# Performance work log

Measured on AMD Instinct MI355X. Metric: run time of the kernel, lower is better.

The kernel has to match this reference:

```python
import jax, jax.numpy as jnp
import numpy as np

B, S, D, H, G = 4, 2048, 1024, 16, 32
HD = D // H
LN_EPS = 1e-5


def _lin_init(key, fan_in, fan_out):
    kw, kb = jax.random.split(key)
    bound = 1.0 / np.sqrt(fan_in)
    W = jax.random.uniform(kw, (fan_in, fan_out), jnp.float32, -bound, bound)
    b = jax.random.uniform(kb, (fan_out,), jnp.float32, -bound, bound)
    return W, b


def setup_inputs() -> dict:
    key = jax.random.key(0)
    ks = jax.random.split(key, 9)
    x = jax.random.normal(ks[0], (B, S, D), jnp.float32)
    geo_features = jax.random.normal(ks[1], (B, G), jnp.float32)
    Wq, bq = _lin_init(ks[2], D, D)
    Wk, bk = _lin_init(ks[3], D, D)
    Wv, bv = _lin_init(ks[4], D, D)
    Wo, bo = _lin_init(ks[5], D, D)
    ge_W1, ge_b1 = _lin_init(ks[6], G, D)
    ln_g = jnp.ones((D,), jnp.float32)
    ln_b = jnp.zeros((D,), jnp.float32)
    ge_W2, ge_b2 = _lin_init(ks[7], D, D)
    gm_W, gm_b = _lin_init(ks[8], D, H)
    return dict(x=x, geo_features=geo_features, Wq=Wq, bq=bq, Wk=Wk, bk=bk,
                Wv=Wv, bv=bv, Wo=Wo, bo=bo, ge_W1=ge_W1, ge_b1=ge_b1,
                ln_g=ln_g, ln_b=ln_b, ge_W2=ge_W2, ge_b2=ge_b2,
                gm_W=gm_W, gm_b=gm_b)


def reference(x, geo_features, Wq, bq, Wk, bk, Wv, bv, Wo, bo,
              ge_W1, ge_b1, ln_g, ln_b, ge_W2, ge_b2, gm_W, gm_b):
    # QKV projections -> (B, H, S, HD)
    def split_heads(t):
        return t.reshape(B, S, H, HD).transpose(0, 2, 1, 3)
    Q = split_heads(x @ Wq + bq)
    K = split_heads(x @ Wk + bk)
    V = split_heads(x @ Wv + bv)

    # geo encoder: Linear -> LayerNorm -> ReLU -> Linear
    h = geo_features @ ge_W1 + ge_b1                      # (B, D)
    mu = jnp.mean(h, axis=-1, keepdims=True)
    var = jnp.mean(jnp.square(h - mu), axis=-1, keepdims=True)
    h = (h - mu) / jnp.sqrt(var + LN_EPS) * ln_g + ln_b
    h = jax.nn.relu(h)
    geo_encoded = h @ ge_W2 + ge_b2                       # (B, D)
    geo_mod = jax.nn.sigmoid(geo_encoded @ gm_W + gm_b)   # (B, H)

    scale = 1.0 / np.sqrt(HD)
    scores = jnp.einsum('bhqd,bhkd->bhqk', Q, K) * scale  # (B, H, S, S)
    scores = scores * (1.0 + geo_mod[:, :, None, None])
    attn = jax.nn.softmax(scores, axis=-1)                # dropout in eval mode: identity
    ctx = jnp.einsum('bhqk,bhkd->bhqd', attn, V)          # (B, H, S, HD)
    ctx = ctx.transpose(0, 2, 1, 3).reshape(B, S, D)
    out = ctx @ Wo + bo
    return out, attn
```

## Files before the change

kernel.cpp:

```cpp
#include <hip/hip_runtime.h>

typedef __attribute__((ext_vector_type(8))) short bf16x8;
typedef __attribute__((ext_vector_type(4))) float f32x4;
typedef __attribute__((ext_vector_type(4))) unsigned short us4;
typedef unsigned short u16;

#define MB (1024*1024)

#define WAITV(N) asm volatile("s_waitcnt vmcnt(" #N ")" ::: "memory")
#define WAITL0() asm volatile("s_waitcnt lgkmcnt(0)" ::: "memory")
#define BAR()    __builtin_amdgcn_s_barrier()
#define SCHEDB() __builtin_amdgcn_sched_barrier(0)

__device__ __forceinline__ u16 f2bf(float f) {
    unsigned u = __float_as_uint(f);
    unsigned r = (u + 0x7fffu + ((u >> 16) & 1u)) >> 16;
    return (u16)r;
}

__device__ __forceinline__ unsigned cvtpk(float a, float b) {
    unsigned r;
    asm("v_cvt_pk_bf16_f32 %0, %1, %2" : "=v"(r) : "v"(a), "v"(b));
    return r;
}

__device__ __forceinline__ f32x4 mfma16(bf16x8 a, bf16x8 b, f32x4 c) {
    return __builtin_amdgcn_mfma_f32_16x16x32_bf16(a, b, c, 0, 0, 0);
}

__device__ __forceinline__ void gload16(const void* g, void* l) {
    __builtin_amdgcn_global_load_lds(
        (__attribute__((address_space(1))) void*)(unsigned long long)g,
        (__attribute__((address_space(3))) void*)l, 16, 0, 0);
}

__global__ __launch_bounds__(256) void k_cvtx(const float* __restrict__ x, u16* __restrict__ xb) {
    const long long i = (long long)blockIdx.x * 256 + threadIdx.x;
    const float4* xp = (const float4*)x;
    float4 a = xp[i*2], b = xp[i*2+1];
    bf16x8 o;
    o[0]=(short)f2bf(a.x); o[1]=(short)f2bf(a.y); o[2]=(short)f2bf(a.z); o[3]=(short)f2bf(a.w);
    o[4]=(short)f2bf(b.x); o[5]=(short)f2bf(b.y); o[6]=(short)f2bf(b.z); o[7]=(short)f2bf(b.w);
    *(bf16x8*)&xb[i*8] = o;
}

__global__ __launch_bounds__(256) void k_wtcvt(const float* __restrict__ W0, const float* __restrict__ W1,
                                               const float* __restrict__ W2, const float* __restrict__ W3,
                                               u16* __restrict__ wt) {
    __shared__ float tl[32][33];
    const int t = threadIdx.x, z = blockIdx.z;
    const float* W = (z==0)?W0:(z==1)?W1:(z==2)?W2:W3;
    const int k0 = blockIdx.x*32, n0 = blockIdx.y*32;
    const int r = t >> 3, c4 = (t & 7) * 4;
    float4 v = *(const float4*)&W[(long long)(k0+r)*1024 + n0 + c4];
    tl[r][c4] = v.x; tl[r][c4+1] = v.y; tl[r][c4+2] = v.z; tl[r][c4+3] = v.w;
    __syncthreads();
    us4 ov;
    ov[0] = f2bf(tl[c4+0][r]); ov[1] = f2bf(tl[c4+1][r]);
    ov[2] = f2bf(tl[c4+2][r]); ov[3] = f2bf(tl[c4+3][r]);
    *(us4*)&wt[((long long)z << 20) + (long long)(n0+r)*1024 + k0 + c4] = ov;
}

__global__ __launch_bounds__(1024) void k_geo1(const float* __restrict__ geo, const float* __restrict__ W1,
                                               const float* __restrict__ b1, const float* __restrict__ lng,
                                               const float* __restrict__ lnb, float* __restrict__ hr) {
    const int b = blockIdx.x, j = threadIdx.x;
    float acc = b1[j];
    #pragma unroll 8
    for (int g = 0; g < 32; ++g) acc += geo[b*32+g] * W1[(long long)g*1024 + j];
    float s1 = acc, s2 = acc*acc;
    #pragma unroll
    for (int m = 1; m < 64; m <<= 1) { s1 += __shfl_xor(s1, m); s2 += __shfl_xor(s2, m); }
    __shared__ float r1[16], r2[16];
    __shared__ float mu_s, rv_s;
    const int wid = threadIdx.x >> 6, lid = threadIdx.x & 63;
    if (lid == 0) { r1[wid] = s1; r2[wid] = s2; }
    __syncthreads();
    if (threadIdx.x == 0) {
        float S1 = 0.f, S2 = 0.f;
        for (int i = 0; i < 16; ++i) { S1 += r1[i]; S2 += r2[i]; }
        float mu = S1 / 1024.f;
        float var = S2 / 1024.f - mu*mu;
        mu_s = mu; rv_s = rsqrtf(var + 1e-5f);
    }
    __syncthreads();
    float hv = (acc - mu_s) * rv_s * lng[j] + lnb[j];
    hr[b*1024 + j] = fmaxf(hv, 0.f);
}

__global__ __launch_bounds__(256) void k_geo2(const float* __restrict__ hr, const float* __restrict__ W2,
                                              const float* __restrict__ b2, float* __restrict__ ge) {
    const int b = blockIdx.x >> 2;
    const int j = (blockIdx.x & 3)*256 + threadIdx.x;
    __shared__ float hs[1024];
    #pragma unroll
    for (int i = 0; i < 4; ++i) hs[threadIdx.x*4 + i] = hr[b*1024 + threadIdx.x*4 + i];
    __syncthreads();
    float acc = b2[j];
    #pragma unroll 8
    for (int d = 0; d < 1024; ++d) acc += hs[d] * W2[(long long)d*1024 + j];
    ge[b*1024 + j] = acc;
}

__global__ __launch_bounds__(64) void k_geo3(const float* __restrict__ ge, const float* __restrict__ gmW,
                                             const float* __restrict__ gmb, float* __restrict__ qs) {
    const int t = threadIdx.x;
    const int b = t >> 4, hh = t & 15;
    float acc = gmb[hh];
    #pragma unroll 8
    for (int d = 0; d < 1024; ++d) acc += ge[b*1024 + d] * gmW[d*16 + hh];
    qs[t] = 0.125f * (1.f + 1.f/(1.f + __expf(-acc)));
}

__global__ __launch_bounds__(256) void k_qkv_gemm(const u16* __restrict__ xb, const u16* __restrict__ wtq,
                                                  const float* __restrict__ bq, const float* __restrict__ bk,
                                                  const float* __restrict__ bv, u16* __restrict__ outq) {
    __shared__ u16 lA[128*64];
    __shared__ u16 lB[128*64];
    const int t = threadIdx.x, z = blockIdx.z;
    const int m0 = blockIdx.y * 128, n0 = blockIdx.x * 128;
    const u16* wt = wtq + (long long)z * (1024*1024);
    const float* bias = (z==0) ? bq : (z==1) ? bk : bv;
    u16* out = outq + (long long)z * 8388608;
    const int w = t >> 6, l = t & 63, lm = l & 15, lg = l >> 4;
    const int wr = (w >> 1) * 64, wc = (w & 1) * 64;
    f32x4 acc[4][4] = {};
    const char* gA = (const char*)xb + (long long)(m0 + (t>>3))*2048 + (t&7)*16;
    const char* gB = (const char*)wt + (long long)(n0 + (t>>3))*2048 + (t&7)*16;
    char* lAp = (char*)lA + t*16;
    char* lBp = (char*)lB + t*16;
    for (int k0 = 0; k0 < 1024; k0 += 64) {
        #pragma unroll
        for (int i = 0; i < 4; ++i) {
            gload16(gA + (long long)i*32*2048, lAp + i*4096);
            gload16(gB + (long long)i*32*2048, lBp + i*4096);
        }
        gA += 128; gB += 128;
        __syncthreads();
        #pragma unroll
        for (int kk = 0; kk < 2; ++kk) {
            bf16x8 af[4], bfr[4];
            #pragma unroll
            for (int mi = 0; mi < 4; ++mi)
                af[mi] = *(const bf16x8*)((const char*)lA + (wr + mi*16 + lm)*128 + kk*64 + lg*16);
            #pragma unroll
            for (int ni = 0; ni < 4; ++ni)
                bfr[ni] = *(const bf16x8*)((const char*)lB + (wc + ni*16 + lm)*128 + kk*64 + lg*16);
            #pragma unroll
            for (int mi = 0; mi < 4; ++mi)
                #pragma unroll
                for (int ni = 0; ni < 4; ++ni)
                    acc[mi][ni] = mfma16(af[mi], bfr[ni], acc[mi][ni]);
        }
        __syncthreads();
    }
    #pragma unroll
    for (int ni = 0; ni < 4; ++ni) {
        const int n = n0 + wc + ni*16 + lm;
        const float bn = bias[n];
        const int hh = n >> 6, d = n & 63;
        #pragma unroll
        for (int mi = 0; mi < 4; ++mi) {
            #pragma unroll
            for (int r = 0; r < 4; ++r) {
                const int m = m0 + wr + mi*16 + lg*4 + r;
                const int b = m >> 11, s = m & 2047;
                out[(((long long)b*16 + hh)*2048 + s)*64 + d] = f2bf(acc[mi][ni][r] + bn);
            }
        }
    }
}

__global__ __launch_bounds__(256) void k_vtrans(const u16* __restrict__ vb, u16* __restrict__ vt) {
    __shared__ u16 tl[64][40];
    const int t = threadIdx.x;
    const int bh = blockIdx.z, s0 = blockIdx.y*64, d0 = blockIdx.x*32;
    const u16* vsrc = vb + (long long)bh*2048*64;
    {
        const int sl = t >> 2, dg = t & 3;
        bf16x8 v = *(const bf16x8*)&vsrc[(long long)(s0+sl)*64 + d0 + dg*8];
        *(bf16x8*)&tl[sl][dg*8] = v;
    }
    __syncthreads();
    {
        const int dl = t >> 3, sg = t & 7;
        bf16x8 o;
        #pragma unroll
        for (int j = 0; j < 8; ++j) o[j] = (short)tl[sg*8+j][dl];
        *(bf16x8*)&vt[((long long)bh*64 + d0+dl)*2048 + s0 + sg*8] = o;
    }
}

__global__ __launch_bounds__(256, 3) void k_attn(const u16* __restrict__ Qb, const u16* __restrict__ Kb,
                                                 const u16* __restrict__ Vt, const float* __restrict__ qsv,
                                                 float* __restrict__ attn_out, u16* __restrict__ ctxb) {
    __shared__ char lds[49152];

    const int nl = blockIdx.x;
    const int ob = (nl & 7)*128 + (nl >> 3);
    const int bh = ob >> 4, qt = ob & 15;
    const int t = threadIdx.x, w = t >> 6, l = t & 63, lm = l & 15, lg = l >> 4;
    const int q0 = qt * 128;
    const float qs = qsv[bh];

    const char* KB = (const char*)Kb + (long long)bh * 262144;
    const char* VB = (const char*)Vt + (long long)bh * 262144;

    bf16x8 qf[2][2];
    {
        const char* QB = (const char*)Qb + (long long)bh * 262144;
        #pragma unroll
        for (int ms = 0; ms < 2; ++ms)
            #pragma unroll
            for (int kc = 0; kc < 2; ++kc)
                qf[ms][kc] = *(const bf16x8*)(QB + (long long)(q0 + w*32 + ms*16 + lm)*128 + kc*64 + lg*16);
    }

    int offA[2], srcK[2], srcV[2];
    #pragma unroll
    for (int i = 0; i < 2; ++i) {
        const int off = i*4096 + t*16;
        const int row = off >> 7, cb = off & 127;
        offA[i] = off;
        srcK[i] = row*128  + (cb ^ ((row & 7) << 4));
        srcV[i] = row*4096 + (cb ^ ((row & 7) << 4));
    }

    float lsum[2] = {0.f, 0.f};
    {
        #pragma unroll
        for (int i = 0; i < 2; ++i) gload16(KB + srcK[i], lds + offA[i]);
        #pragma unroll
        for (int i = 0; i < 2; ++i) gload16(KB + 8192 + srcK[i], lds + 8192 + offA[i]);
        SCHEDB();
        WAITV(2); BAR(); SCHEDB();

        int cb_ = 0, sb_ = 2;
        for (int kt = 0; kt < 32; ++kt) {
            const int ktn = (kt < 30) ? kt + 2 : 31;
            {
                char* dst = lds + sb_*8192;
                #pragma unroll
                for (int i = 0; i < 2; ++i)
                    gload16(KB + (long long)ktn*8192 + srcK[i], dst + offA[i]);
            }
            SCHEDB();
            const char* kb = lds + cb_*8192;
            #pragma unroll
            for (int ns = 0; ns < 4; ++ns) {
                const int rowb = ns*16 + lm;
                const int tag = (rowb & 7) << 4;
                bf16x8 kf0 = *(const bf16x8*)(kb + rowb*128 + ((lg*16) ^ tag));
                bf16x8 kf1 = *(const bf16x8*)(kb + rowb*128 + ((64 + lg*16) ^ tag));
                #pragma unroll
                for (int ms = 0; ms < 2; ++ms) {
                    f32x4 a = {};
                    a = mfma16(kf0, qf[ms][0], a);
                    a = mfma16(kf1, qf[ms][1], a);
                    lsum[ms] += __expf(a[0]*qs) + __expf(a[1]*qs)
                              + __expf(a[2]*qs) + __expf(a[3]*qs);
                }
            }
            WAITV(2); BAR(); SCHEDB();
            cb_ = (cb_ == 2) ? 0 : cb_ + 1;
            sb_ = (sb_ == 2) ? 0 : sb_ + 1;
        }
    }
    WAITV(0); BAR(); SCHEDB();

    float invl[2];
    #pragma unroll
    for (int ms = 0; ms < 2; ++ms) {
        float v = lsum[ms];
        v += __shfl_xor(v, 16);
        v += __shfl_xor(v, 32);
        invl[ms] = 1.f / v;
    }

    char* lP = lds + 32768;
    float* aL = attn_out + ((long long)bh*2048 + q0 + w*32 + lm)*2048 + lg*4;
    f32x4 cacc[2][4] = {};

    {
        #pragma unroll
        for (int i = 0; i < 2; ++i) gload16(KB + srcK[i], lds + offA[i]);
        #pragma unroll
        for (int i = 0; i < 2; ++i) gload16(VB + srcV[i], lds + 16384 + offA[i]);
        SCHEDB();
        WAITV(0); BAR(); SCHEDB();

        for (int kt = 0; kt < 32; ++kt) {
            const int cur = kt & 1, nxt = cur ^ 1;
            const int ktn = (kt < 31) ? kt + 1 : 31;
            {
                char* dK = lds + nxt*8192;
                char* dV = lds + 16384 + nxt*8192;
                #pragma unroll
                for (int i = 0; i < 2; ++i)
                    gload16(KB + (long long)ktn*8192 + srcK[i], dK + offA[i]);
                #pragma unroll
                for (int i = 0; i < 2; ++i)
                    gload16(VB + (long long)ktn*128 + srcV[i], dV + offA[i]);
            }
            SCHEDB();

            const char* kb = lds + cur*8192;
            #pragma unroll
            for (int ns = 0; ns < 4; ++ns) {
                const int rowb = ns*16 + lm;
                const int tag = (rowb & 7) << 4;
                bf16x8 kf0 = *(const bf16x8*)(kb + rowb*128 + ((lg*16) ^ tag));
                bf16x8 kf1 = *(const bf16x8*)(kb + rowb*128 + ((64 + lg*16) ^ tag));
                #pragma unroll
                for (int ms = 0; ms < 2; ++ms) {
                    f32x4 a = {};
                    a = mfma16(kf0, qf[ms][0], a);
                    a = mfma16(kf1, qf[ms][1], a);
                    const float p0 = __expf(a[0]*qs) * invl[ms];
                    const float p1 = __expf(a[1]*qs) * invl[ms];
                    const float p2 = __expf(a[2]*qs) * invl[ms];
                    const float p3 = __expf(a[3]*qs) * invl[ms];
                    f32x4 pv4 = {p0, p1, p2, p3};
                    __builtin_nontemporal_store(pv4, (f32x4*)(aL + ms*32768 + kt*64 + ns*16));
                    const int prow = w*32 + ms*16 + lm;
                    const int ptag = (prow & 7) << 4;
                    uint2 pk; pk.x = cvtpk(p0, p1); pk.y = cvtpk(p2, p3);
                    *(uint2*)(lP + prow*128 + ((32*ns + 8*lg) ^ ptag)) = pk;
                }
            }
            WAITL0(); SCHEDB();

            const char* vb = lds + 16384 + cur*8192;
            #pragma unroll
            for (int ks = 0; ks < 2; ++ks) {
                bf16x8 pa[2];
                #pragma unroll
                for (int ms = 0; ms < 2; ++ms) {
                    const int prow = w*32 + ms*16 + lm;
                    pa[ms] = *(const bf16x8*)(lP + prow*128 + ((ks*64 + lg*16) ^ ((prow & 7) << 4)));
                }
                #pragma unroll
                for (int dn = 0; dn < 4; ++dn) {
                    const int rv = dn*16 + lm;
                    bf16x8 vf = *(const bf16x8*)(vb + rv*128 + ((ks*64 + lg*16) ^ ((rv & 7) << 4)));
                    cacc[0][dn] = mfma16(pa[0], vf, cacc[0][dn]);
                    cacc[1][dn] = mfma16(pa[1], vf, cacc[1][dn]);
                }
            }
            WAITV(8); BAR(); SCHEDB();
        }
    }

    const int b = bh >> 4, hh = bh & 15;
    #pragma unroll
    for (int ms = 0; ms < 2; ++ms)
        #pragma unroll
        for (int dn = 0; dn < 4; ++dn)
            #pragma unroll
            for (int r = 0; r < 4; ++r) {
                const int q = q0 + w*32 + ms*16 + lg*4 + r;
                ctxb[(((long long)b*2048 + q)*16 + hh)*64 + dn*16 + lm] = f2bf(cacc[ms][dn][r]);
            }
}

__global__ __launch_bounds__(256) void k_o_gemm(const u16* __restrict__ ab, const u16* __restrict__ wt,
                                                const float* __restrict__ bo, float* __restrict__ outf) {
    __shared__ u16 lA[128*64];
    __shared__ u16 lB[128*64];
    const int t = threadIdx.x;
    const int m0 = blockIdx.y * 128, n0 = blockIdx.x * 128;
    const int w = t >> 6, l = t & 63, lm = l & 15, lg = l >> 4;
    const int wr = (w >> 1) * 64, wc = (w & 1) * 64;
    f32x4 acc[4][4] = {};
    const char* gA = (const char*)ab + (long long)(m0 + (t>>3))*2048 + (t&7)*16;
    const char* gB = (const char*)wt + (long long)(n0 + (t>>3))*2048 + (t&7)*16;
    char* lAp = (char*)lA + t*16;
    char* lBp = (char*)lB + t*16;
    for (int k0 = 0; k0 < 1024; k0 += 64) {
        #pragma unroll
        for (int i = 0; i < 4; ++i) {
            gload16(gA + (long long)i*32*2048, lAp + i*4096);
            gload16(gB + (long long)i*32*2048, lBp + i*4096);
        }
        gA += 128; gB += 128;
        __syncthreads();
        #pragma unroll
        for (int kk = 0; kk < 2; ++kk) {
            bf16x8 af[4], bfr[4];
            #pragma unroll
            for (int mi = 0; mi < 4; ++mi)
                af[mi] = *(const bf16x8*)((const char*)lA + (wr + mi*16 + lm)*128 + kk*64 + lg*16);
            #pragma unroll
            for (int ni = 0; ni < 4; ++ni)
                bfr[ni] = *(const bf16x8*)((const char*)lB + (wc + ni*16 + lm)*128 + kk*64 + lg*16);
            #pragma unroll
            for (int mi = 0; mi < 4; ++mi)
                #pragma unroll
                for (int ni = 0; ni < 4; ++ni)
                    acc[mi][ni] = mfma16(af[mi], bfr[ni], acc[mi][ni]);
        }
        __syncthreads();
    }
    #pragma unroll
    for (int ni = 0; ni < 4; ++ni) {
        const int n = n0 + wc + ni*16 + lm;
        const float bn = bo[n];
        #pragma unroll
        for (int mi = 0; mi < 4; ++mi) {
            #pragma unroll
            for (int r = 0; r < 4; ++r) {
                const int m = m0 + wr + mi*16 + lg*4 + r;
                outf[(long long)m*1024 + n] = acc[mi][ni][r] + bn;
            }
        }
    }
}

extern "C" void kernel_launch(void* const* d_in, const int* in_sizes, int n_in,
                              void* d_out, int out_size, void* d_ws, size_t ws_size,
                              hipStream_t stream) {
    const float* x    = (const float*)d_in[0];
    const float* geo  = (const float*)d_in[1];
    const float* Wq   = (const float*)d_in[2];
    const float* bq   = (const float*)d_in[3];
    const float* Wk   = (const float*)d_in[4];
    const float* bk   = (const float*)d_in[5];
    const float* Wv   = (const float*)d_in[6];
    const float* bv   = (const float*)d_in[7];
    const float* Wo   = (const float*)d_in[8];
    const float* bo   = (const float*)d_in[9];
    const float* geW1 = (const float*)d_in[10];
    const float* geb1 = (const float*)d_in[11];
    const float* lng  = (const float*)d_in[12];
    const float* lnb  = (const float*)d_in[13];
    const float* geW2 = (const float*)d_in[14];
    const float* geb2 = (const float*)d_in[15];
    const float* gmW  = (const float*)d_in[16];
    const float* gmb  = (const float*)d_in[17];

    char* ws = (char*)d_ws;
    u16* xb   = (u16*)(ws + 0);
    u16* wt   = (u16*)(ws + 16*(size_t)MB);
    u16* qkv  = (u16*)(ws + 24*(size_t)MB);
    u16* Qb   = qkv;
    u16* Kb   = (u16*)(ws + 40*(size_t)MB);
    u16* Vb   = (u16*)(ws + 56*(size_t)MB);
    u16* Vt   = (u16*)(ws + 72*(size_t)MB);
    u16* ctx  = Vb;
    float* hr = (float*)(ws + 88*(size_t)MB);
    float* ge = (float*)(ws + 88*(size_t)MB + 65536);
    float* qsb= (float*)(ws + 88*(size_t)MB + 131072);

    float* outf = (float*)d_out;
    float* attn = outf + 8388608;

    hipLaunchKernelGGL(k_cvtx,    dim3(4096),      dim3(256),  0, stream, x, xb);
    hipLaunchKernelGGL(k_wtcvt,   dim3(32,32,4),   dim3(256),  0, stream, Wq, Wk, Wv, Wo, wt);
    hipLaunchKernelGGL(k_geo1,    dim3(4),         dim3(1024), 0, stream, geo, geW1, geb1, lng, lnb, hr);
    hipLaunchKernelGGL(k_geo2,    dim3(16),        dim3(256),  0, stream, hr, geW2, geb2, ge);
    hipLaunchKernelGGL(k_geo3,    dim3(1),         dim3(64),   0, stream, ge, gmW, gmb, qsb);
    hipLaunchKernelGGL(k_qkv_gemm,dim3(8,64,3),    dim3(256),  0, stream, xb, wt, bq, bk, bv, qkv);
    hipLaunchKernelGGL(k_vtrans,  dim3(2,32,64),   dim3(256),  0, stream, Vb, Vt);
    hipLaunchKernelGGL(k_attn,    dim3(1024),      dim3(256),  0, stream, Qb, Kb, Vt, qsb, attn, ctx);
    hipLaunchKernelGGL(k_o_gemm,  dim3(8,64),      dim3(256),  0, stream, ctx, wt + 3*1048576, bo, outf);
}
```

Baseline: 580.7 us.

## Widen attention blocks to 512 threads covering 256 query rows

Each attention block now has 8 waves covering 256 query rows instead of 4 waves covering 128, so each K/V tile staged in LDS is shared by twice as many queries. The grid is halved, and each thread now issues one 16-byte async load per tile instead of two. LDS grows to 64KB to hold the extra per-wave P staging. The launch bound (512,4) requests high occupancy, which may force a tight VGPR budget and cause spills, and 64KB of LDS per block limits how many blocks fit on a CU.

New measurement: 583.1 us. About the same (+0.4%).

```diff
diff --git a/kernel.cpp b/kernel.cpp
--- a/kernel.cpp
+++ b/kernel.cpp
@@ -191,16 +191,16 @@
     }
 }
 
-__global__ __launch_bounds__(256, 3) void k_attn(const u16* __restrict__ Qb, const u16* __restrict__ Kb,
+__global__ __launch_bounds__(512, 4) void k_attn(const u16* __restrict__ Qb, const u16* __restrict__ Kb,
                                                  const u16* __restrict__ Vt, const float* __restrict__ qsv,
                                                  float* __restrict__ attn_out, u16* __restrict__ ctxb) {
-    __shared__ char lds[49152];
+    __shared__ char lds[65536];
 
     const int nl = blockIdx.x;
-    const int ob = (nl & 7)*128 + (nl >> 3);
-    const int bh = ob >> 4, qt = ob & 15;
+    const int ob = (nl & 7)*64 + (nl >> 3);
+    const int bh = ob >> 3, qt = ob & 7;
     const int t = threadIdx.x, w = t >> 6, l = t & 63, lm = l & 15, lg = l >> 4;
-    const int q0 = qt * 128;
+    const int q0 = qt * 256;
     const float qs = qsv[bh];
 
     const char* KB = (const char*)Kb + (long long)bh * 262144;
@@ -216,34 +216,23 @@
                 qf[ms][kc] = *(const bf16x8*)(QB + (long long)(q0 + w*32 + ms*16 + lm)*128 + kc*64 + lg*16);
     }
 
-    int offA[2], srcK[2], srcV[2];
-    #pragma unroll
-    for (int i = 0; i < 2; ++i) {
-        const int off = i*4096 + t*16;
-        const int row = off >> 7, cb = off & 127;
-        offA[i] = off;
-        srcK[i] = row*128  + (cb ^ ((row & 7) << 4));
-        srcV[i] = row*4096 + (cb ^ ((row & 7) << 4));
-    }
+    const int off = t*16;
+    const int row = off >> 7, cb = off & 127;
+    const int offA = off;
+    const int srcK = row*128  + (cb ^ ((row & 7) << 4));
+    const int srcV = row*4096 + (cb ^ ((row & 7) << 4));
 
     float lsum[2] = {0.f, 0.f};
     {
-        #pragma unroll
-        for (int i = 0; i < 2; ++i) gload16(KB + srcK[i], lds + offA[i]);
-        #pragma unroll
-        for (int i = 0; i < 2; ++i) gload16(KB + 8192 + srcK[i], lds + 8192 + offA[i]);
+        gload16(KB + srcK, lds + offA);
+        gload16(KB + 8192 + srcK, lds + 8192 + offA);
         SCHEDB();
-        WAITV(2); BAR(); SCHEDB();
+        WAITV(1); BAR(); SCHEDB();
 
         int cb_ = 0, sb_ = 2;
         for (int kt = 0; kt < 32; ++kt) {
             const int ktn = (kt < 30) ? kt + 2 : 31;
-            {
-                char* dst = lds + sb_*8192;
-                #pragma unroll
-                for (int i = 0; i < 2; ++i)
-                    gload16(KB + (long long)ktn*8192 + srcK[i], dst + offA[i]);
-            }
+            gload16(KB + (long long)ktn*8192 + srcK, lds + sb_*8192 + offA);
             SCHEDB();
             const char* kb = lds + cb_*8192;
             #pragma unroll
@@ -261,7 +250,7 @@
                               + __expf(a[2]*qs) + __expf(a[3]*qs);
                 }
             }
-            WAITV(2); BAR(); SCHEDB();
+            WAITV(1); BAR(); SCHEDB();
             cb_ = (cb_ == 2) ? 0 : cb_ + 1;
             sb_ = (sb_ == 2) ? 0 : sb_ + 1;
         }
@@ -282,26 +271,16 @@
     f32x4 cacc[2][4] = {};
 
     {
-        #pragma unroll
-        for (int i = 0; i < 2; ++i) gload16(KB + srcK[i], lds + offA[i]);
-        #pragma unroll
-        for (int i = 0; i < 2; ++i) gload16(VB + srcV[i], lds + 16384 + offA[i]);
+        gload16(KB + srcK, lds + offA);
+        gload16(VB + srcV, lds + 16384 + offA);
         SCHEDB();
         WAITV(0); BAR(); SCHEDB();
 
         for (int kt = 0; kt < 32; ++kt) {
             const int cur = kt & 1, nxt = cur ^ 1;
             const int ktn = (kt < 31) ? kt + 1 : 31;
-            {
-                char* dK = lds + nxt*8192;
-                char* dV = lds + 16384 + nxt*8192;
-                #pragma unroll
-                for (int i = 0; i < 2; ++i)
-                    gload16(KB + (long long)ktn*8192 + srcK[i], dK + offA[i]);
-                #pragma unroll
-                for (int i = 0; i < 2; ++i)
-                    gload16(VB + (long long)ktn*128 + srcV[i], dV + offA[i]);
-            }
+            gload16(KB + (long long)ktn*8192 + srcK, lds + nxt*8192 + offA);
+            gload16(VB + (long long)ktn*128 + srcV, lds + 16384 + nxt*8192 + offA);
             SCHEDB();
 
             const char* kb = lds + cur*8192;
@@ -461,6 +440,6 @@
     hipLaunchKernelGGL(k_geo3,    dim3(1),         dim3(64),   0, stream, ge, gmW, gmb, qsb);
     hipLaunchKernelGGL(k_qkv_gemm,dim3(8,64,3),    dim3(256),  0, stream, xb, wt, bq, bk, bv, qkv);
     hipLaunchKernelGGL(k_vtrans,  dim3(2,32,64),   dim3(256),  0, stream, Vb, Vt);
-    hipLaunchKernelGGL(k_attn,    dim3(1024),      dim3(256),  0, stream, Qb, Kb, Vt, qsb, attn, ctx);
+    hipLaunchKernelGGL(k_attn,    dim3(512),       dim3(512),  0, stream, Qb, Kb, Vt, qsb, attn, ctx);
     hipLaunchKernelGGL(k_o_gemm,  dim3(8,64),      dim3(256),  0, stream, ctx, wt + 3*1048576, bo, outf);
 }
```
